# Optimization experiments

Hardware: AMD Instinct MI355X
Metric: run time of the kernel (lower is better)

Reference implementation:

```python
import jax, jax.numpy as jnp
import numpy as np

B, S, D, H, K = 2, 2048, 1024, 16, 16


def setup_inputs() -> dict:
    key = jax.random.key(0)
    ks = jax.random.split(key, 8)
    s = 0.02
    def w(k, shape):
        return s * jax.random.normal(k, shape, jnp.float32)
    return {
        "x": jax.random.normal(ks[0], (B, S, D), jnp.float32),
        "Wq": w(ks[1], (D, D)), "bq": jnp.zeros((D,), jnp.float32),
        "Wk": w(ks[2], (D, D)), "bk": jnp.zeros((D,), jnp.float32),
        "Wv": w(ks[3], (D, D)), "bv": jnp.zeros((D,), jnp.float32),
        "Wo": w(ks[4], (D, D)), "bo": jnp.zeros((D,), jnp.float32),
        "Ws1": w(ks[5], (D, D // 2)), "bs1": jnp.zeros((D // 2,), jnp.float32),
        "Ws2": w(ks[6], (D // 2, 1)), "bs2": jnp.zeros((1,), jnp.float32),
    }


def reference(x, Wq, bq, Wk, bk, Wv, bv, Wo, bo, Ws1, bs1, Ws2, bs2):
    Bx, Sx, Dx = x.shape
    Dh = Dx // H
    # QKV projections -> [B, H, S, Dh]
    q = (x @ Wq + bq).reshape(Bx, Sx, H, Dh).transpose(0, 2, 1, 3)
    k = (x @ Wk + bk).reshape(Bx, Sx, H, Dh).transpose(0, 2, 1, 3)
    v = (x @ Wv + bv).reshape(Bx, Sx, H, Dh).transpose(0, 2, 1, 3)
    scores = jnp.einsum('bhqd,bhkd->bhqk', q, k) / np.float32(np.sqrt(Dh))
    # Lightning-indexer importance: [B, S]; identical across heads, so compute once.
    imp = jax.nn.sigmoid(jax.nn.relu(x @ Ws1 + bs1) @ Ws2 + bs2)[..., 0]
    _, idx = jax.lax.top_k(imp, K)  # [B, K]
    sel = jnp.zeros((Bx, Sx), bool).at[jnp.arange(Bx)[:, None], idx].set(True)
    # sparse mask: position (i, j) kept if row i OR column j is a top-k token
    m2 = sel[:, :, None] | sel[:, None, :]  # [B, S, S]
    masked = jnp.where(m2[:, None, :, :], scores, -jnp.inf)
    w = jax.nn.softmax(masked, axis=-1)
    att = jnp.einsum('bhqk,bhkd->bhqd', w, v).transpose(0, 2, 1, 3).reshape(Bx, Sx, Dx)
    return att @ Wo + bo
```

## Files before the change

### kernel.cpp

```cpp
#include <hip/hip_runtime.h>
#include <math.h>

constexpr int Bb = 2, Ss = 2048, Dd = 1024, Hh = 16, Kk = 16;

typedef __bf16 bf16x8 __attribute__((ext_vector_type(8)));
typedef __bf16 bf16x4 __attribute__((ext_vector_type(4)));
typedef float  f32x4  __attribute__((ext_vector_type(4)));

__device__ __forceinline__ void gld_lds16(const void* g, void* l) {
    __builtin_amdgcn_global_load_lds(
        (const __attribute__((address_space(1))) unsigned int*)g,
        (__attribute__((address_space(3))) unsigned int*)l, 16, 0, 0);
}

__device__ __forceinline__ unsigned fmap(float f) {
    unsigned u = __float_as_uint(f);
    return (u & 0x80000000u) ? ~u : (u | 0x80000000u);
}
__device__ __forceinline__ float funmap(unsigned u) {
    return (u & 0x80000000u) ? __uint_as_float(u ^ 0x80000000u) : __uint_as_float(~u);
}

__global__ void __launch_bounds__(256) gemm_qkv_ind(
    const __bf16* __restrict__ xb, const __bf16* __restrict__ xlo,
    const __bf16* __restrict__ WqT, const __bf16* __restrict__ WkT,
    const __bf16* __restrict__ WvT,
    const float* __restrict__ bq, const float* __restrict__ bk,
    const float* __restrict__ bv,
    __bf16* __restrict__ qb, __bf16* __restrict__ kb, __bf16* __restrict__ vb,
    const __bf16* __restrict__ W1Th, const __bf16* __restrict__ W1Tl,
    const float* __restrict__ bs1, const float* __restrict__ Ws2,
    float* __restrict__ imp)
{
    __shared__ __bf16 sm[12288];

    const int t    = threadIdx.x;
    const int wave = t >> 6;
    const int lane = t & 63;
    const int bm   = blockIdx.y * 128;
    const int fr   = lane & 15;
    const int fq   = lane >> 4;
    const int K    = Dd;
    const int z    = blockIdx.z;

    if (z < 3) {
        const __bf16* BT  = (z == 0) ? WqT : (z == 1) ? WkT : WvT;
        const float* bias = (z == 0) ? bq  : (z == 1) ? bk  : bv;
        __bf16*      C    = (z == 0) ? qb  : (z == 1) ? kb  : vb;
        __bf16* As = sm;
        __bf16* Bs = sm + 4096;

        const int bn = blockIdx.x * 128;
        const int wm = (wave & 1) * 64;
        const int wn = (wave >> 1) * 64;

        f32x4 acc[4][4] = {};

        for (int k0 = 0; k0 < K; k0 += 32) {
            #pragma unroll
            for (int l = 0; l < 2; ++l) {
                int c = l * 256 + t;
                const __bf16* ga = xb + (size_t)(bm + (c >> 2)) * K + k0 + (c & 3) * 8;
                gld_lds16(ga, As + (size_t)(l * 256 + wave * 64) * 8);
                const __bf16* gb = BT + (size_t)(bn + (c >> 2)) * K + k0 + (c & 3) * 8;
                gld_lds16(gb, Bs + (size_t)(l * 256 + wave * 64) * 8);
            }
            __syncthreads();

            bf16x8 af[4], bf[4];
            #pragma unroll
            for (int i = 0; i < 4; ++i)
                af[i] = *(const bf16x8*)(As + (wm + i * 16 + fr) * 32 + fq * 8);
            #pragma unroll
            for (int j = 0; j < 4; ++j)
                bf[j] = *(const bf16x8*)(Bs + (wn + j * 16 + fr) * 32 + fq * 8);
            #pragma unroll
            for (int i = 0; i < 4; ++i)
                #pragma unroll
                for (int j = 0; j < 4; ++j)
                    acc[i][j] = __builtin_amdgcn_mfma_f32_16x16x32_bf16(af[i], bf[j], acc[i][j], 0, 0, 0);
            __syncthreads();
        }

        const int cr = (lane >> 4) * 4;
        const int cc = lane & 15;
        #pragma unroll
        for (int j = 0; j < 4; ++j) {
            int col = bn + wn + j * 16 + cc;
            float bb = bias[col];
            #pragma unroll
            for (int i = 0; i < 4; ++i) {
                #pragma unroll
                for (int r = 0; r < 4; ++r)
                    C[(size_t)(bm + wm + i * 16 + cr + r) * Dd + col] =
                        (__bf16)(acc[i][j][r] + bb);
            }
        }
    } else {
        __bf16* Ah = sm;
        __bf16* Al = sm + 4096;
        __bf16* Bh = sm + 8192;
        __bf16* Bl = sm + 10240;

        const int bn = blockIdx.x * 64;
        const int wm = (wave & 1) * 64;
        const int wn = (wave >> 1) * 32;

        f32x4 acc[4][2] = {};

        for (int k0 = 0; k0 < K; k0 += 32) {
            #pragma unroll
            for (int l = 0; l < 2; ++l) {
                int c = l * 256 + t;
                size_t goff = (size_t)(bm + (c >> 2)) * K + k0 + (c & 3) * 8;
                gld_lds16(xb  + goff, Ah + (size_t)(l * 256 + wave * 64) * 8);
                gld_lds16(xlo + goff, Al + (size_t)(l * 256 + wave * 64) * 8);
            }
            {
                int c = t;
                size_t goff = (size_t)(bn + (c >> 2)) * K + k0 + (c & 3) * 8;
                gld_lds16(W1Th + goff, Bh + (size_t)(wave * 64) * 8);
                gld_lds16(W1Tl + goff, Bl + (size_t)(wave * 64) * 8);
            }
            __syncthreads();

            bf16x8 ah[4], al[4], bh[2], bl[2];
            #pragma unroll
            for (int i = 0; i < 4; ++i) {
                ah[i] = *(const bf16x8*)(Ah + (wm + i * 16 + fr) * 32 + fq * 8);
                al[i] = *(const bf16x8*)(Al + (wm + i * 16 + fr) * 32 + fq * 8);
            }
            #pragma unroll
            for (int j = 0; j < 2; ++j) {
                bh[j] = *(const bf16x8*)(Bh + (wn + j * 16 + fr) * 32 + fq * 8);
                bl[j] = *(const bf16x8*)(Bl + (wn + j * 16 + fr) * 32 + fq * 8);
            }
            #pragma unroll
            for (int i = 0; i < 4; ++i)
                #pragma unroll
                for (int j = 0; j < 2; ++j) {
                    acc[i][j] = __builtin_amdgcn_mfma_f32_16x16x32_bf16(al[i], bh[j], acc[i][j], 0, 0, 0);
                    acc[i][j] = __builtin_amdgcn_mfma_f32_16x16x32_bf16(ah[i], bl[j], acc[i][j], 0, 0, 0);
                    acc[i][j] = __builtin_amdgcn_mfma_f32_16x16x32_bf16(ah[i], bh[j], acc[i][j], 0, 0, 0);
                }
            __syncthreads();
        }

        const int cr = (lane >> 4) * 4;
        const int cc = lane & 15;
        float bb[2], w2[2];
        #pragma unroll
        for (int j = 0; j < 2; ++j) {
            int col = bn + wn + j * 16 + cc;
            bb[j] = bs1[col];
            w2[j] = Ws2[col];
        }
        #pragma unroll
        for (int i = 0; i < 4; ++i) {
            #pragma unroll
            for (int r = 0; r < 4; ++r) {
                float vsum = fmaxf(acc[i][0][r] + bb[0], 0.f) * w2[0]
                           + fmaxf(acc[i][1][r] + bb[1], 0.f) * w2[1];
                #pragma unroll
                for (int off = 8; off > 0; off >>= 1)
                    vsum += __shfl_xor(vsum, off, 16);
                if (cc == 0)
                    atomicAdd(imp + (bm + wm + i * 16 + cr + r), vsum);
            }
        }
    }
}

__global__ void __launch_bounds__(256) gemm_out(
    const __bf16* __restrict__ A, const __bf16* __restrict__ BT,
    const float* __restrict__ bias, float* __restrict__ C, int M, int N, int K)
{
    __shared__ __bf16 As[128 * 32];
    __shared__ __bf16 Bs[128 * 32];

    const int t    = threadIdx.x;
    const int wave = t >> 6;
    const int lane = t & 63;
    const int bm   = blockIdx.y * 128;
    const int bn   = blockIdx.x * 128;
    const int wm   = (wave & 1) * 64;
    const int wn   = (wave >> 1) * 64;
    const int fr   = lane & 15;
    const int fq   = lane >> 4;

    f32x4 acc[4][4] = {};

    for (int k0 = 0; k0 < K; k0 += 32) {
        #pragma unroll
        for (int l = 0; l < 2; ++l) {
            int c = l * 256 + t;
            const __bf16* ga = A + (size_t)(bm + (c >> 2)) * K + k0 + (c & 3) * 8;
            gld_lds16(ga, As + (size_t)(l * 256 + wave * 64) * 8);
            const __bf16* gb = BT + (size_t)(bn + (c >> 2)) * K + k0 + (c & 3) * 8;
            gld_lds16(gb, Bs + (size_t)(l * 256 + wave * 64) * 8);
        }
        __syncthreads();

        bf16x8 af[4], bf[4];
        #pragma unroll
        for (int i = 0; i < 4; ++i)
            af[i] = *(const bf16x8*)(As + (wm + i * 16 + fr) * 32 + fq * 8);
        #pragma unroll
        for (int j = 0; j < 4; ++j)
            bf[j] = *(const bf16x8*)(Bs + (wn + j * 16 + fr) * 32 + fq * 8);
        #pragma unroll
        for (int i = 0; i < 4; ++i)
            #pragma unroll
            for (int j = 0; j < 4; ++j)
                acc[i][j] = __builtin_amdgcn_mfma_f32_16x16x32_bf16(af[i], bf[j], acc[i][j], 0, 0, 0);
        __syncthreads();
    }

    const int cr = (lane >> 4) * 4;
    const int cc = lane & 15;
    #pragma unroll
    for (int j = 0; j < 4; ++j) {
        int col = bn + wn + j * 16 + cc;
        float bb = bias[col];
        #pragma unroll
        for (int i = 0; i < 4; ++i) {
            #pragma unroll
            for (int r = 0; r < 4; ++r)
                C[(size_t)(bm + wm + i * 16 + cr + r) * N + col] = acc[i][j][r] + bb;
        }
    }
}

__global__ void __launch_bounds__(256) pack_x_hilo(
    const float* __restrict__ src, __bf16* __restrict__ hi, __bf16* __restrict__ lo,
    float* __restrict__ imp, float* __restrict__ oacc,
    float* __restrict__ lsum, unsigned* __restrict__ macc)
{
    int i = blockIdx.x * 256 + threadIdx.x;
    if (i < Bb * Ss) imp[i] = 0.f;
    if (i < Bb * Hh * Kk * 64) oacc[i] = 0.f;
    if (i < Bb * Hh * Kk) { lsum[i] = 0.f; macc[i] = 0u; }
    float4 v = ((const float4*)src)[i];
    bf16x4 h = { (__bf16)v.x, (__bf16)v.y, (__bf16)v.z, (__bf16)v.w };
    bf16x4 l = { (__bf16)(v.x - (float)h[0]), (__bf16)(v.y - (float)h[1]),
                 (__bf16)(v.z - (float)h[2]), (__bf16)(v.w - (float)h[3]) };
    ((bf16x4*)hi)[i] = h;
    ((bf16x4*)lo)[i] = l;
}

__global__ void __launch_bounds__(256) transpose_all(
    const float* __restrict__ W0, const float* __restrict__ W1,
    const float* __restrict__ W2, const float* __restrict__ W3,
    __bf16* __restrict__ T0, __bf16* __restrict__ T1,
    __bf16* __restrict__ T2, __bf16* __restrict__ T3,
    const float* __restrict__ Ws1, __bf16* __restrict__ Th, __bf16* __restrict__ Tl)
{
    __shared__ float tile[32][33];
    int tx = threadIdx.x & 31, ty = threadIdx.x >> 5;
    int n0 = blockIdx.x * 32, k0 = blockIdx.y * 32;
    int z = blockIdx.z;

    if (z < 4) {
        const float* W = (z == 0) ? W0 : (z == 1) ? W1 : (z == 2) ? W2 : W3;
        __bf16*      T = (z == 0) ? T0 : (z == 1) ? T1 : (z == 2) ? T2 : T3;
        #pragma unroll
        for (int i = 0; i < 32; i += 8)
            tile[ty + i][tx] = W[(size_t)(k0 + ty + i) * 1024 + n0 + tx];
        __syncthreads();
        #pragma unroll
        for (int i = 0; i < 32; i += 8)
            T[(size_t)(n0 + ty + i) * 1024 + k0 + tx] = (__bf16)tile[tx][ty + i];
    } else {
        if (blockIdx.x >= 16) return;
        #pragma unroll
        for (int i = 0; i < 32; i += 8)
            tile[ty + i][tx] = Ws1[(size_t)(k0 + ty + i) * 512 + n0 + tx];
        __syncthreads();
        #pragma unroll
        for (int i = 0; i < 32; i += 8) {
            float v = tile[tx][ty + i];
            __bf16 h = (__bf16)v;
            Th[(size_t)(n0 + ty + i) * 1024 + k0 + tx] = h;
            Tl[(size_t)(n0 + ty + i) * 1024 + k0 + tx] = (__bf16)(v - (float)h);
        }
    }
}

__global__ void __launch_bounds__(256) topk_kernel(
    const float* __restrict__ imp, int* __restrict__ sel_idx)
{
    int b = blockIdx.x;
    int t = threadIdx.x;
    __shared__ float vals[Ss];
    __shared__ float sv[256];
    __shared__ int   si[256];

    for (int j = t; j < Ss; j += 256) vals[j] = imp[b * Ss + j];
    __syncthreads();

    for (int it = 0; it < Kk; ++it) {
        float best = -1e30f; int bidx = 0x7fffffff;
        for (int j = t; j < Ss; j += 256) {
            float v = vals[j];
            if (v > best || (v == best && j < bidx)) { best = v; bidx = j; }
        }
        sv[t] = best; si[t] = bidx;
        __syncthreads();
        for (int off = 128; off > 0; off >>= 1) {
            if (t < off) {
                float ov = sv[t + off]; int oi = si[t + off];
                if (ov > sv[t] || (ov == sv[t] && oi < si[t])) { sv[t] = ov; si[t] = oi; }
            }
            __syncthreads();
        }
        if (t == 0) {
            sel_idx[b * Kk + it] = si[0];
            vals[si[0]] = -1e30f;
        }
        __syncthreads();
    }
}

__global__ void __launch_bounds__(256) attn_sparse(
    const __bf16* __restrict__ q, const __bf16* __restrict__ k,
    const __bf16* __restrict__ v, const int* __restrict__ sel_idx,
    __bf16* __restrict__ att)
{
    const int b  = blockIdx.z;
    const int h  = blockIdx.y;
    const int q0 = blockIdx.x * 16;
    const int t  = threadIdx.x;

    __shared__ float KT[64][17];
    __shared__ float Vs[16][64];
    __shared__ float qsh[16][65];
    __shared__ float wsh[16][16];
    __shared__ int   sj[16];

    if (t < 16) sj[t] = sel_idx[b * Kk + t];
    __syncthreads();

    {
        int row = t >> 4, d0 = (t & 15) * 4;
        bf16x4 kv = *(const bf16x4*)(k + ((size_t)(b * Ss + sj[row])) * Dd + h * 64 + d0);
        bf16x4 vv = *(const bf16x4*)(v + ((size_t)(b * Ss + sj[row])) * Dd + h * 64 + d0);
        bf16x4 qv = *(const bf16x4*)(q + ((size_t)(b * Ss + q0 + row)) * Dd + h * 64 + d0);
        #pragma unroll
        for (int i = 0; i < 4; ++i) {
            KT[d0 + i][row]  = (float)kv[i];
            Vs[row][d0 + i]  = (float)vv[i];
            qsh[row][d0 + i] = (float)qv[i];
        }
    }
    __syncthreads();

    const int wave = t >> 6, lane = t & 63;
    const int ql = lane >> 4, j = lane & 15;
    const int qi = wave * 4 + ql;

    float s = 0.f;
    #pragma unroll
    for (int d = 0; d < 64; ++d) s = fmaf(qsh[qi][d], KT[d][j], s);
    s *= 0.125f;

    float m = s;
    #pragma unroll
    for (int off = 8; off > 0; off >>= 1) m = fmaxf(m, __shfl_xor(m, off, 16));
    float e = __expf(s - m);
    float sum = e;
    #pragma unroll
    for (int off = 8; off > 0; off >>= 1) sum += __shfl_xor(sum, off, 16);
    wsh[qi][j] = e / sum;

    #pragma unroll
    for (int q2 = 0; q2 < 4; ++q2) {
        int qq = wave * 4 + q2;
        float o = 0.f;
        #pragma unroll
        for (int jj = 0; jj < 16; ++jj)
            o = fmaf(wsh[qq][jj], Vs[jj][lane], o);
        att[((size_t)(b * Ss + q0 + qq)) * Dd + h * 64 + lane] = (__bf16)o;
    }
}

__global__ void __launch_bounds__(256) attn_dense_qk(
    const __bf16* __restrict__ q, const __bf16* __restrict__ k,
    const int* __restrict__ sel_idx, float* __restrict__ Sbuf,
    unsigned* __restrict__ macc)
{
    const int b  = blockIdx.z, h = blockIdx.y, j0 = blockIdx.x * 128;
    const int t  = threadIdx.x;

    __shared__ float Ks[128][65];
    __shared__ float Qs[16][65];

    #pragma unroll
    for (int l = 0; l < 4; ++l) {
        int c = t + 256 * l;
        int row = c >> 3, seg = c & 7;
        bf16x8 kv = *(const bf16x8*)(k + ((size_t)(b * Ss + j0 + row)) * Dd + h * 64 + seg * 8);
        #pragma unroll
        for (int e = 0; e < 8; ++e) Ks[row][seg * 8 + e] = (float)kv[e];
    }
    if (t < 128) {
        int row = t >> 3, seg = t & 7;
        int i = sel_idx[b * Kk + row];
        bf16x8 qv = *(const bf16x8*)(q + ((size_t)(b * Ss + i)) * Dd + h * 64 + seg * 8);
        #pragma unroll
        for (int e = 0; e < 8; ++e) Qs[row][seg * 8 + e] = (float)qv[e];
    }
    __syncthreads();

    const int qi = t >> 4, ks = t & 15;
    const int bhq = (b * Hh + h) * Kk + qi;
    float lmax = -1e30f;
    #pragma unroll
    for (int s8 = 0; s8 < 8; ++s8) {
        int j = ks + s8 * 16;
        float s = 0.f;
        #pragma unroll
        for (int d = 0; d < 64; ++d) s = fmaf(Qs[qi][d], Ks[j][d], s);
        s *= 0.125f;
        Sbuf[(size_t)bhq * Ss + j0 + j] = s;
        lmax = fmaxf(lmax, s);
    }
    #pragma unroll
    for (int off = 8; off > 0; off >>= 1) lmax = fmaxf(lmax, __shfl_xor(lmax, off, 16));
    if (ks == 0) atomicMax(macc + bhq, fmap(lmax));
}

__global__ void __launch_bounds__(256) attn_dense_pv(
    const __bf16* __restrict__ v, const float* __restrict__ Sbuf,
    const unsigned* __restrict__ macc, float* __restrict__ lsum,
    float* __restrict__ oacc)
{
    const int b  = blockIdx.z, h = blockIdx.y, j0 = blockIdx.x * 128;
    const int t  = threadIdx.x;

    __shared__ float Vs[128][64];
    __shared__ float Es[16][144];

    #pragma unroll
    for (int l = 0; l < 4; ++l) {
        int c = t + 256 * l;
        int row = c >> 3, seg = c & 7;
        bf16x8 vv = *(const bf16x8*)(v + ((size_t)(b * Ss + j0 + row)) * Dd + h * 64 + seg * 8);
        #pragma unroll
        for (int e = 0; e < 8; ++e) Vs[row][seg * 8 + e] = (float)vv[e];
    }

    const int qi = t >> 4, ks = t & 15;
    const int bhq = (b * Hh + h) * Kk + qi;
    const float mq = funmap(macc[bhq]);
    float psum = 0.f;
    #pragma unroll
    for (int s8 = 0; s8 < 8; ++s8) {
        int j = ks + s8 * 16;
        float e = __expf(Sbuf[(size_t)bhq * Ss + j0 + j] - mq);
        Es[qi][j] = e;
        psum += e;
    }
    #pragma unroll
    for (int off = 8; off > 0; off >>= 1) psum += __shfl_xor(psum, off, 16);
    if (ks == 0) atomicAdd(lsum + bhq, psum);
    __syncthreads();

    const int d = t & 63, qg = t >> 6;
    #pragma unroll
    for (int qq = 0; qq < 4; ++qq) {
        int qx = qg * 4 + qq;
        float o = 0.f;
        #pragma unroll 4
        for (int jj = 0; jj < 128; ++jj)
            o = fmaf(Es[qx][jj], Vs[jj][d], o);
        atomicAdd(oacc + (size_t)((b * Hh + h) * Kk + qx) * 64 + d, o);
    }
}

__global__ void __launch_bounds__(64) attn_dense_fin(
    const float* __restrict__ oacc, const float* __restrict__ lsum,
    const int* __restrict__ sel_idx, __bf16* __restrict__ att)
{
    int bid = blockIdx.x;
    int qi = bid & 15, h = (bid >> 4) & 15, b = bid >> 8;
    int bhq = (b * Hh + h) * Kk + qi;
    int i = sel_idx[b * Kk + qi];
    float val = oacc[(size_t)bhq * 64 + threadIdx.x] / lsum[bhq];
    att[((size_t)(b * Ss + i)) * Dd + h * 64 + threadIdx.x] = (__bf16)val;
}

extern "C" void kernel_launch(void* const* d_in, const int* in_sizes, int n_in,
                              void* d_out, int out_size, void* d_ws, size_t ws_size,
                              hipStream_t stream)
{
    const float* x   = (const float*)d_in[0];
    const float* Wq  = (const float*)d_in[1];
    const float* bq  = (const float*)d_in[2];
    const float* Wk  = (const float*)d_in[3];
    const float* bk  = (const float*)d_in[4];
    const float* Wv  = (const float*)d_in[5];
    const float* bv  = (const float*)d_in[6];
    const float* Wo  = (const float*)d_in[7];
    const float* bo  = (const float*)d_in[8];
    const float* Ws1 = (const float*)d_in[9];
    const float* bs1 = (const float*)d_in[10];
    const float* Ws2 = (const float*)d_in[11];
    float* out = (float*)d_out;

    const size_t MSD = (size_t)Bb * Ss * Dd;
    const int M = Bb * Ss;

    char* p = (char*)d_ws;
    __bf16* qb  = (__bf16*)p; p += MSD * sizeof(__bf16);
    __bf16* kb  = (__bf16*)p; p += MSD * sizeof(__bf16);
    __bf16* vb  = (__bf16*)p; p += MSD * sizeof(__bf16);
    __bf16* att = (__bf16*)p; p += MSD * sizeof(__bf16);
    __bf16* xb  = (__bf16*)p; p += MSD * sizeof(__bf16);
    __bf16* xlo = (__bf16*)p; p += MSD * sizeof(__bf16);
    __bf16* WqT = (__bf16*)p; p += (size_t)Dd * Dd * sizeof(__bf16);
    __bf16* WkT = (__bf16*)p; p += (size_t)Dd * Dd * sizeof(__bf16);
    __bf16* WvT = (__bf16*)p; p += (size_t)Dd * Dd * sizeof(__bf16);
    __bf16* WoT = (__bf16*)p; p += (size_t)Dd * Dd * sizeof(__bf16);
    __bf16* W1Th = (__bf16*)p; p += (size_t)512 * Dd * sizeof(__bf16);
    __bf16* W1Tl = (__bf16*)p; p += (size_t)512 * Dd * sizeof(__bf16);
    float* imp  = (float*)p; p += (size_t)Bb * Ss * sizeof(float);
    int* sel_idx = (int*)p; p += (size_t)Bb * Kk * sizeof(int);
    float* oacc = (float*)p; p += (size_t)Bb * Hh * Kk * 64 * sizeof(float);
    float* lsum = (float*)p; p += (size_t)Bb * Hh * Kk * sizeof(float);
    unsigned* macc = (unsigned*)p; p += (size_t)Bb * Hh * Kk * sizeof(unsigned);
    float* Sbuf = (float*)xlo;

    pack_x_hilo<<<dim3((int)(MSD / 4 / 256)), 256, 0, stream>>>(
        x, xb, xlo, imp, oacc, lsum, macc);
    transpose_all<<<dim3(32, 32, 5), 256, 0, stream>>>(
        Wq, Wk, Wv, Wo, WqT, WkT, WvT, WoT, Ws1, W1Th, W1Tl);
    gemm_qkv_ind<<<dim3(8, 32, 4), 256, 0, stream>>>(
        xb, xlo, WqT, WkT, WvT, bq, bk, bv, qb, kb, vb,
        W1Th, W1Tl, bs1, Ws2, imp);
    topk_kernel<<<dim3(Bb), 256, 0, stream>>>(imp, sel_idx);
    attn_sparse<<<dim3(Ss / 16, Hh, Bb), 256, 0, stream>>>(qb, kb, vb, sel_idx, att);
    attn_dense_qk<<<dim3(Ss / 128, Hh, Bb), 256, 0, stream>>>(qb, kb, sel_idx, Sbuf, macc);
    attn_dense_pv<<<dim3(Ss / 128, Hh, Bb), 256, 0, stream>>>(vb, Sbuf, macc, lsum, oacc);
    attn_dense_fin<<<dim3(Bb * Hh * Kk), 64, 0, stream>>>(oacc, lsum, sel_idx, att);
    gemm_out<<<dim3(8, 32), 256, 0, stream>>>(att, WoT, bo, out, M, Dd, Dd);
}
```

Measured before the change: 267.7 us.

## Swizzle LDS tiles, deepen K-step, merge prep kernels, reshape output GEMM grid

The QKV and output GEMMs move to a K-step of 64 with an XOR-swizzled LDS layout, which is meant to avoid bank conflicts and halve the number of barriers. The indexer GEMM gets the same swizzle on its 32-wide tiles. The output GEMM switches to 64x128 tiles, doubling the block count so more CUs are busy. The x hi/lo packing and the weight transposes are fused into one prep launch. The QKV grid is flattened with the z index interleaved, so the four GEMM variants are spread across the machine. These changes add LDS use and index arithmetic.

```diff
diff --git a/kernel.cpp b/kernel.cpp
--- a/kernel.cpp
+++ b/kernel.cpp
@@ -32,53 +32,64 @@
     const float* __restrict__ bs1, const float* __restrict__ Ws2,
     float* __restrict__ imp)
 {
-    __shared__ __bf16 sm[12288];
-
+    __shared__ __bf16 sm[16384];
+
+    const int bid  = blockIdx.x;
+    const int z    = bid & 3;
+    const int rid  = bid >> 2;
+    const int bxi  = rid & 7;
+    const int bm   = (rid >> 3) * 128;
     const int t    = threadIdx.x;
     const int wave = t >> 6;
     const int lane = t & 63;
-    const int bm   = blockIdx.y * 128;
     const int fr   = lane & 15;
     const int fq   = lane >> 4;
     const int K    = Dd;
-    const int z    = blockIdx.z;
 
     if (z < 3) {
         const __bf16* BT  = (z == 0) ? WqT : (z == 1) ? WkT : WvT;
         const float* bias = (z == 0) ? bq  : (z == 1) ? bk  : bv;
         __bf16*      C    = (z == 0) ? qb  : (z == 1) ? kb  : vb;
         __bf16* As = sm;
-        __bf16* Bs = sm + 4096;
-
-        const int bn = blockIdx.x * 128;
+        __bf16* Bs = sm + 8192;
+
+        const int bn = bxi * 128;
         const int wm = (wave & 1) * 64;
         const int wn = (wave >> 1) * 64;
 
         f32x4 acc[4][4] = {};
 
-        for (int k0 = 0; k0 < K; k0 += 32) {
-            #pragma unroll
-            for (int l = 0; l < 2; ++l) {
+        for (int k0 = 0; k0 < K; k0 += 64) {
+            #pragma unroll
+            for (int l = 0; l < 4; ++l) {
                 int c = l * 256 + t;
-                const __bf16* ga = xb + (size_t)(bm + (c >> 2)) * K + k0 + (c & 3) * 8;
-                gld_lds16(ga, As + (size_t)(l * 256 + wave * 64) * 8);
-                const __bf16* gb = BT + (size_t)(bn + (c >> 2)) * K + k0 + (c & 3) * 8;
-                gld_lds16(gb, Bs + (size_t)(l * 256 + wave * 64) * 8);
+                int row = c >> 3, seg = (c & 7) ^ (row & 7);
+                gld_lds16(xb + (size_t)(bm + row) * K + k0 + seg * 8,
+                          As + (size_t)(l * 256 + wave * 64) * 8);
+                gld_lds16(BT + (size_t)(bn + row) * K + k0 + seg * 8,
+                          Bs + (size_t)(l * 256 + wave * 64) * 8);
             }
             __syncthreads();
 
-            bf16x8 af[4], bf[4];
-            #pragma unroll
-            for (int i = 0; i < 4; ++i)
-                af[i] = *(const bf16x8*)(As + (wm + i * 16 + fr) * 32 + fq * 8);
-            #pragma unroll
-            for (int j = 0; j < 4; ++j)
-                bf[j] = *(const bf16x8*)(Bs + (wn + j * 16 + fr) * 32 + fq * 8);
-            #pragma unroll
-            for (int i = 0; i < 4; ++i)
-                #pragma unroll
-                for (int j = 0; j < 4; ++j)
-                    acc[i][j] = __builtin_amdgcn_mfma_f32_16x16x32_bf16(af[i], bf[j], acc[i][j], 0, 0, 0);
+            #pragma unroll
+            for (int s = 0; s < 2; ++s) {
+                bf16x8 af[4], bf[4];
+                #pragma unroll
+                for (int i = 0; i < 4; ++i) {
+                    int row = wm + i * 16 + fr;
+                    af[i] = *(const bf16x8*)(As + row * 64 + (((s * 4 + fq) ^ (row & 7)) * 8));
+                }
+                #pragma unroll
+                for (int j = 0; j < 4; ++j) {
+                    int row = wn + j * 16 + fr;
+                    bf[j] = *(const bf16x8*)(Bs + row * 64 + (((s * 4 + fq) ^ (row & 7)) * 8));
+                }
+                #pragma unroll
+                for (int i = 0; i < 4; ++i)
+                    #pragma unroll
+                    for (int j = 0; j < 4; ++j)
+                        acc[i][j] = __builtin_amdgcn_mfma_f32_16x16x32_bf16(af[i], bf[j], acc[i][j], 0, 0, 0);
+            }
             __syncthreads();
         }
 
@@ -102,7 +113,7 @@
         __bf16* Bh = sm + 8192;
         __bf16* Bl = sm + 10240;
 
-        const int bn = blockIdx.x * 64;
+        const int bn = bxi * 64;
         const int wm = (wave & 1) * 64;
         const int wn = (wave >> 1) * 32;
 
@@ -112,13 +123,15 @@
             #pragma unroll
             for (int l = 0; l < 2; ++l) {
                 int c = l * 256 + t;
-                size_t goff = (size_t)(bm + (c >> 2)) * K + k0 + (c & 3) * 8;
+                int row = c >> 2, seg = (c & 3) ^ (row & 3);
+                size_t goff = (size_t)(bm + row) * K + k0 + seg * 8;
                 gld_lds16(xb  + goff, Ah + (size_t)(l * 256 + wave * 64) * 8);
                 gld_lds16(xlo + goff, Al + (size_t)(l * 256 + wave * 64) * 8);
             }
             {
                 int c = t;
-                size_t goff = (size_t)(bn + (c >> 2)) * K + k0 + (c & 3) * 8;
+                int row = c >> 2, seg = (c & 3) ^ (row & 3);
+                size_t goff = (size_t)(bn + row) * K + k0 + seg * 8;
                 gld_lds16(W1Th + goff, Bh + (size_t)(wave * 64) * 8);
                 gld_lds16(W1Tl + goff, Bl + (size_t)(wave * 64) * 8);
             }
@@ -127,13 +140,17 @@
             bf16x8 ah[4], al[4], bh[2], bl[2];
             #pragma unroll
             for (int i = 0; i < 4; ++i) {
-                ah[i] = *(const bf16x8*)(Ah + (wm + i * 16 + fr) * 32 + fq * 8);
-                al[i] = *(const bf16x8*)(Al + (wm + i * 16 + fr) * 32 + fq * 8);
+                int row = wm + i * 16 + fr;
+                int off = row * 32 + ((fq ^ (row & 3)) * 8);
+                ah[i] = *(const bf16x8*)(Ah + off);
+                al[i] = *(const bf16x8*)(Al + off);
             }
             #pragma unroll
             for (int j = 0; j < 2; ++j) {
-                bh[j] = *(const bf16x8*)(Bh + (wn + j * 16 + fr) * 32 + fq * 8);
-                bl[j] = *(const bf16x8*)(Bl + (wn + j * 16 + fr) * 32 + fq * 8);
+                int row = wn + j * 16 + fr;
+                int off = row * 32 + ((fq ^ (row & 3)) * 8);
+                bh[j] = *(const bf16x8*)(Bh + off);
+                bl[j] = *(const bf16x8*)(Bl + off);
             }
             #pragma unroll
             for (int i = 0; i < 4; ++i)
@@ -175,44 +192,57 @@
     const __bf16* __restrict__ A, const __bf16* __restrict__ BT,
     const float* __restrict__ bias, float* __restrict__ C, int M, int N, int K)
 {
-    __shared__ __bf16 As[128 * 32];
-    __shared__ __bf16 Bs[128 * 32];
+    __shared__ __bf16 As[64 * 64];
+    __shared__ __bf16 Bs[128 * 64];
 
     const int t    = threadIdx.x;
     const int wave = t >> 6;
     const int lane = t & 63;
-    const int bm   = blockIdx.y * 128;
+    const int bm   = blockIdx.y * 64;
     const int bn   = blockIdx.x * 128;
-    const int wm   = (wave & 1) * 64;
+    const int wm   = (wave & 1) * 32;
     const int wn   = (wave >> 1) * 64;
     const int fr   = lane & 15;
     const int fq   = lane >> 4;
 
-    f32x4 acc[4][4] = {};
-
-    for (int k0 = 0; k0 < K; k0 += 32) {
+    f32x4 acc[2][4] = {};
+
+    for (int k0 = 0; k0 < K; k0 += 64) {
         #pragma unroll
         for (int l = 0; l < 2; ++l) {
             int c = l * 256 + t;
-            const __bf16* ga = A + (size_t)(bm + (c >> 2)) * K + k0 + (c & 3) * 8;
-            gld_lds16(ga, As + (size_t)(l * 256 + wave * 64) * 8);
-            const __bf16* gb = BT + (size_t)(bn + (c >> 2)) * K + k0 + (c & 3) * 8;
-            gld_lds16(gb, Bs + (size_t)(l * 256 + wave * 64) * 8);
+            int row = c >> 3, seg = (c & 7) ^ (row & 7);
+            gld_lds16(A + (size_t)(bm + row) * K + k0 + seg * 8,
+                      As + (size_t)(l * 256 + wave * 64) * 8);
+        }
+        #pragma unroll
+        for (int l = 0; l < 4; ++l) {
+            int c = l * 256 + t;
+            int row = c >> 3, seg = (c & 7) ^ (row & 7);
+            gld_lds16(BT + (size_t)(bn + row) * K + k0 + seg * 8,
+                      Bs + (size_t)(l * 256 + wave * 64) * 8);
         }
         __syncthreads();
 
-        bf16x8 af[4], bf[4];
-        #pragma unroll
-        for (int i = 0; i < 4; ++i)
-            af[i] = *(const bf16x8*)(As + (wm + i * 16 + fr) * 32 + fq * 8);
-        #pragma unroll
-        for (int j = 0; j < 4; ++j)
-            bf[j] = *(const bf16x8*)(Bs + (wn + j * 16 + fr) * 32 + fq * 8);
-        #pragma unroll
-        for (int i = 0; i < 4; ++i)
-            #pragma unroll
-            for (int j = 0; j < 4; ++j)
-                acc[i][j] = __builtin_amdgcn_mfma_f32_16x16x32_bf16(af[i], bf[j], acc[i][j], 0, 0, 0);
+        #pragma unroll
+        for (int s = 0; s < 2; ++s) {
+            bf16x8 af[2], bf[4];
+            #pragma unroll
+            for (int i = 0; i < 2; ++i) {
+                int row = wm + i * 16 + fr;
+                af[i] = *(const bf16x8*)(As + row * 64 + (((s * 4 + fq) ^ (row & 7)) * 8));
+            }
+            #pragma unroll
+            for (int j = 0; j < 4; ++j) {
+                int row = wn + j * 16 + fr;
+                bf[j] = *(const bf16x8*)(Bs + row * 64 + (((s * 4 + fq) ^ (row & 7)) * 8));
+            }
+            #pragma unroll
+            for (int i = 0; i < 2; ++i)
+                #pragma unroll
+                for (int j = 0; j < 4; ++j)
+                    acc[i][j] = __builtin_amdgcn_mfma_f32_16x16x32_bf16(af[i], bf[j], acc[i][j], 0, 0, 0);
+        }
         __syncthreads();
     }
 
@@ -223,7 +253,7 @@
         int col = bn + wn + j * 16 + cc;
         float bb = bias[col];
         #pragma unroll
-        for (int i = 0; i < 4; ++i) {
+        for (int i = 0; i < 2; ++i) {
             #pragma unroll
             for (int r = 0; r < 4; ++r)
                 C[(size_t)(bm + wm + i * 16 + cr + r) * N + col] = acc[i][j][r] + bb;
@@ -231,24 +261,10 @@
     }
 }
 
-__global__ void __launch_bounds__(256) pack_x_hilo(
-    const float* __restrict__ src, __bf16* __restrict__ hi, __bf16* __restrict__ lo,
+__global__ void __launch_bounds__(256) prep_kernel(
+    const float* __restrict__ x, __bf16* __restrict__ hi, __bf16* __restrict__ lo,
     float* __restrict__ imp, float* __restrict__ oacc,
-    float* __restrict__ lsum, unsigned* __restrict__ macc)
-{
-    int i = blockIdx.x * 256 + threadIdx.x;
-    if (i < Bb * Ss) imp[i] = 0.f;
-    if (i < Bb * Hh * Kk * 64) oacc[i] = 0.f;
-    if (i < Bb * Hh * Kk) { lsum[i] = 0.f; macc[i] = 0u; }
-    float4 v = ((const float4*)src)[i];
-    bf16x4 h = { (__bf16)v.x, (__bf16)v.y, (__bf16)v.z, (__bf16)v.w };
-    bf16x4 l = { (__bf16)(v.x - (float)h[0]), (__bf16)(v.y - (float)h[1]),
-                 (__bf16)(v.z - (float)h[2]), (__bf16)(v.w - (float)h[3]) };
-    ((bf16x4*)hi)[i] = h;
-    ((bf16x4*)lo)[i] = l;
-}
-
-__global__ void __launch_bounds__(256) transpose_all(
+    float* __restrict__ lsum, unsigned* __restrict__ macc,
     const float* __restrict__ W0, const float* __restrict__ W1,
     const float* __restrict__ W2, const float* __restrict__ W3,
     __bf16* __restrict__ T0, __bf16* __restrict__ T1,
@@ -256,9 +272,28 @@
     const float* __restrict__ Ws1, __bf16* __restrict__ Th, __bf16* __restrict__ Tl)
 {
     __shared__ float tile[32][33];
+    const int bid = blockIdx.x;
+
+    if (bid < 4096) {
+        int i = bid * 256 + threadIdx.x;
+        if (i < Bb * Ss) imp[i] = 0.f;
+        if (i < Bb * Hh * Kk * 64) oacc[i] = 0.f;
+        if (i < Bb * Hh * Kk) { lsum[i] = 0.f; macc[i] = 0u; }
+        float4 v = ((const float4*)x)[i];
+        bf16x4 h = { (__bf16)v.x, (__bf16)v.y, (__bf16)v.z, (__bf16)v.w };
+        bf16x4 l = { (__bf16)(v.x - (float)h[0]), (__bf16)(v.y - (float)h[1]),
+                     (__bf16)(v.z - (float)h[2]), (__bf16)(v.w - (float)h[3]) };
+        ((bf16x4*)hi)[i] = h;
+        ((bf16x4*)lo)[i] = l;
+        return;
+    }
+
+    int tid = bid - 4096;
+    int z   = tid >> 10;
+    int rem = tid & 1023;
+    int n0  = (rem & 31) * 32;
+    int k0  = (rem >> 5) * 32;
     int tx = threadIdx.x & 31, ty = threadIdx.x >> 5;
-    int n0 = blockIdx.x * 32, k0 = blockIdx.y * 32;
-    int z = blockIdx.z;
 
     if (z < 4) {
         const float* W = (z == 0) ? W0 : (z == 1) ? W1 : (z == 2) ? W2 : W3;
@@ -271,7 +306,7 @@
         for (int i = 0; i < 32; i += 8)
             T[(size_t)(n0 + ty + i) * 1024 + k0 + tx] = (__bf16)tile[tx][ty + i];
     } else {
-        if (blockIdx.x >= 16) return;
+        if (n0 >= 512) return;
         #pragma unroll
         for (int i = 0; i < 32; i += 8)
             tile[ty + i][tx] = Ws1[(size_t)(k0 + ty + i) * 512 + n0 + tx];
@@ -530,11 +565,10 @@
     unsigned* macc = (unsigned*)p; p += (size_t)Bb * Hh * Kk * sizeof(unsigned);
     float* Sbuf = (float*)xlo;
 
-    pack_x_hilo<<<dim3((int)(MSD / 4 / 256)), 256, 0, stream>>>(
-        x, xb, xlo, imp, oacc, lsum, macc);
-    transpose_all<<<dim3(32, 32, 5), 256, 0, stream>>>(
+    prep_kernel<<<dim3(4096 + 5120), 256, 0, stream>>>(
+        x, xb, xlo, imp, oacc, lsum, macc,
         Wq, Wk, Wv, Wo, WqT, WkT, WvT, WoT, Ws1, W1Th, W1Tl);
-    gemm_qkv_ind<<<dim3(8, 32, 4), 256, 0, stream>>>(
+    gemm_qkv_ind<<<dim3(1024), 256, 0, stream>>>(
         xb, xlo, WqT, WkT, WvT, bq, bk, bv, qb, kb, vb,
         W1Th, W1Tl, bs1, Ws2, imp);
     topk_kernel<<<dim3(Bb), 256, 0, stream>>>(imp, sel_idx);
@@ -542,5 +576,5 @@
     attn_dense_qk<<<dim3(Ss / 128, Hh, Bb), 256, 0, stream>>>(qb, kb, sel_idx, Sbuf, macc);
     attn_dense_pv<<<dim3(Ss / 128, Hh, Bb), 256, 0, stream>>>(vb, Sbuf, macc, lsum, oacc);
     attn_dense_fin<<<dim3(Bb * Hh * Kk), 64, 0, stream>>>(oacc, lsum, sel_idx, att);
-    gemm_out<<<dim3(8, 32), 256, 0, stream>>>(att, WoT, bo, out, M, Dd, Dd);
-}
+    gemm_out<<<dim3(8, 64), 256, 0, stream>>>(att, WoT, bo, out, M, Dd, Dd);
+}
```

Measured after the change: 260.8 us. 1.03x faster.
